# Kernel tuning notes

Measured on AMD Instinct MI355X. Metric: run time of the kernel, lower is better.

Reference implementation:

```python
import jax, jax.numpy as jnp
import numpy as np

# --- static config (matches init_kwargs) ---
B = 2048
N_UP, N_DOWN, N_NUC = 16, 14, 8
N_ELEC = N_UP + N_DOWN            # 30
N_ALL = N_ELEC + N_NUC            # 38
BASIS, KD, ED, L = 32, 64, 128, 3
H_K = int(np.round(np.sqrt(BASIS * KD)))  # 45, log-interp hidden dim of kernel MLP
H_O = int(np.round(np.sqrt(KD * ED)))     # 91, log-interp hidden dim of embed_out MLP

# conv_indexing: all (i, j) pairs with j != i  (i over electrons, j over all particles)
_pairs = np.array([(i, j) for i in range(N_ELEC) for j in range(N_ALL) if j != i], dtype=np.int32)
C_I = jnp.asarray(_pairs[:, 0])
C_J = jnp.asarray(_pairs[:, 1])
P = N_ELEC * (N_ALL - 1)


def ssp(x):
    # shifted softplus: log(0.5*exp(x) + 0.5)
    return jax.nn.softplus(x) - jnp.log(2.0).astype(x.dtype)


def setup_inputs() -> dict:
    key = jax.random.key(0)
    ks = jax.random.split(key, 16)
    # spin-shared electron embeddings (one vector per spin channel, expanded)
    up = jax.random.normal(ks[0], (ED,), jnp.float32)
    dn = jax.random.normal(ks[1], (ED,), jnp.float32)
    embedding_elec = jnp.concatenate([jnp.tile(up, (N_UP, 1)), jnp.tile(dn, (N_DOWN, 1))], axis=0)
    s = 0.1  # weight scale for numerical sanity
    inp = {
        'dists_basis': jax.random.uniform(ks[2], (B, N_ELEC, N_ALL, BASIS), jnp.float32),
        'embedding_elec': embedding_elec,
        'embedding_nuc': jax.random.normal(ks[3], (N_NUC, KD), jnp.float32),
        'kernel_w1': s * jax.random.normal(ks[4], (L, BASIS, H_K), jnp.float32),
        'kernel_b1': s * jax.random.normal(ks[5], (L, H_K), jnp.float32),
        'kernel_w2': s * jax.random.normal(ks[6], (L, H_K, KD), jnp.float32),
        'kernel_b2': s * jax.random.normal(ks[7], (L, KD), jnp.float32),
        'embed_in_w': s * jax.random.normal(ks[8], (L, ED, KD), jnp.float32),
        'out_w1': s * jax.random.normal(ks[9], (L, KD, H_O), jnp.float32),
        'out_b1': s * jax.random.normal(ks[10], (L, H_O), jnp.float32),
        'out_w2': s * jax.random.normal(ks[11], (L, H_O, ED), jnp.float32),
        'out_b2': s * jax.random.normal(ks[12], (L, ED), jnp.float32),
    }
    return inp


def reference(dists_basis, embedding_elec, embedding_nuc, kernel_w1, kernel_b1,
              kernel_w2, kernel_b2, embed_in_w, out_w1, out_b1, out_w2, out_b2):
    b = dists_basis.shape[0]
    # gather all (i,j) pair basis features: (B, P, BASIS)
    db = dists_basis[:, C_I, C_J, :]
    xs = jnp.broadcast_to(embedding_elec, (b, N_ELEC, ED))
    nuc = jnp.broadcast_to(embedding_nuc, (b, N_NUC, KD))
    for l in range(L):  # small fixed number of interaction layers
        # kernel MLP on distance basis -> (B, P, KD)
        Ws = ssp(db @ kernel_w1[l] + kernel_b1[l]) @ kernel_w2[l] + kernel_b2[l]
        # embed_in on electrons, concat nuclei embeddings -> (B, N_ALL, KD)
        zs = jnp.concatenate([xs @ embed_in_w[l], nuc], axis=1)
        # gather neighbors, weight, reduce over neighbor axis -> (B, N_ELEC, KD)
        msg = (Ws * zs[:, C_J]).reshape(b, N_ELEC, N_ALL - 1, KD).sum(axis=2)
        # embed_out MLP -> (B, N_ELEC, ED), residual update
        vs = ssp(msg @ out_w1[l] + out_b1[l]) @ out_w2[l] + out_b2[l]
        xs = xs + vs
    return xs
```

## Files before the change

### kernel.cpp

```cpp
#include <hip/hip_runtime.h>
#include <hip/hip_bf16.h>

typedef __attribute__((ext_vector_type(8))) short bf16x8;
typedef __attribute__((ext_vector_type(4))) float f32x4;
typedef __attribute__((ext_vector_type(16))) float f32x16;
typedef __attribute__((ext_vector_type(2))) unsigned int u32x2;

constexpr int NB = 2048;
constexpr int NE = 30, NN = 8, NAll = 38;
constexpr int BAS = 32, KD = 64, ED = 128, HK = 45, HO = 91, LNUM = 3;

#define MFMA32(a, b, c) __builtin_amdgcn_mfma_f32_32x32x16_bf16((a), (b), (c), 0, 0, 0)

__device__ __forceinline__ unsigned cvtpk(float a, float b) {
    unsigned r;
    asm("v_cvt_pk_bf16_f32 %0, %1, %2" : "=v"(r) : "v"(a), "v"(b));
    return r;
}
__device__ __forceinline__ unsigned short f2b(float v) {
    return (unsigned short)cvtpk(v, v);
}
__device__ __forceinline__ bf16x8 cvt8(f32x4 lo, f32x4 hi) {
    union { unsigned u[4]; bf16x8 v; } r;
    r.u[0] = cvtpk(lo[0], lo[1]);
    r.u[1] = cvtpk(lo[2], lo[3]);
    r.u[2] = cvtpk(hi[0], hi[1]);
    r.u[3] = cvtpk(hi[2], hi[3]);
    return r.v;
}
__device__ __forceinline__ float ssp(float x) {
    float e = __expf(-fabsf(x));
    return fmaxf(x, 0.f) + __logf(fmaf(0.5f, e, 0.5f));
}
__device__ __forceinline__ int swzi(int row, int col, int S) {
    int mask = (S >> 3) - 1;
    int blk = ((col >> 3) ^ row) & mask;
    return row * S + (blk << 3) + (col & 7);
}
__device__ __forceinline__ bf16x8 ldfrag(const unsigned short* p, int S, int row, int col) {
    int mask = (S >> 3) - 1;
    int blk = ((col >> 3) ^ row) & mask;
    return *(const bf16x8*)(p + row * S + (blk << 3));
}
__device__ __forceinline__ f32x4 ldf4s(const float* p, int S, int row, int col) {
    int mask = (S >> 3) - 1;
    int blk = ((col >> 3) ^ row) & mask;
    return *(const f32x4*)(p + row * S + (blk << 3) + (col & 7));
}

__global__ __launch_bounds__(256, 4) void schnet_mfma(
    const float* __restrict__ dists,
    const float* __restrict__ emb_e,
    const float* __restrict__ emb_n,
    const float* __restrict__ kw1, const float* __restrict__ kb1,
    const float* __restrict__ kw2, const float* __restrict__ kb2,
    const float* __restrict__ ew,
    const float* __restrict__ ow1, const float* __restrict__ ob1,
    const float* __restrict__ ow2, const float* __restrict__ ob2,
    float* __restrict__ out)
{
    __shared__ __align__(16) unsigned char smem[26368];
    float* zsb  = (float*)smem;
    float* stot = (float*)(smem + 9728);
    unsigned short* w2t = (unsigned short*)(smem + 9984);
    unsigned char* U = smem + 18176;
    float* msgf = (float*)U;
    unsigned short* hobA = (unsigned short*)U;
    unsigned short* hobB = (unsigned short*)(U + 4096);

    const int b = blockIdx.x;
    const int t = threadIdx.x;
    const int l = t & 63, wv = t >> 6;
    const int li = l & 31, hi = l >> 5;
    const float* db_b = dists + (size_t)b * NE * NAll * BAS;
    float* xsg = out + (size_t)b * NE * ED;
    const int ri = (li < NE) ? li : NE - 1;

    const f32x16 z16 = {0,0,0,0,0,0,0,0,0,0,0,0,0,0,0,0};

    for (int o = t; o < NE * ED; o += 256) xsg[o] = emb_e[o];
    for (int o = t; o < NN * KD; o += 256) zsb[NE * KD + o] = emb_n[o];
    __syncthreads();

    for (int lyr = 0; lyr < LNUM; ++lyr) {
        const float* w1g = kw1 + lyr * BAS * HK;
        const float* b1g = kb1 + lyr * HK;
        const float* w2g = kw2 + lyr * HK * KD;
        const float* b2g = kb2 + lyr * KD;
        const float* weg = ew  + lyr * ED * KD;
        const float* o1g = ow1 + lyr * KD * HO;
        const float* g1g = ob1 + lyr * HO;
        const float* o2g = ow2 + lyr * HO * ED;
        const float* g2g = ob2 + lyr * ED;

        for (int o = t; o < 64 * 64; o += 256) {
            int c = o & 63, h = o >> 6;
            w2t[swzi(c, h, 64)] = f2b((h < HK) ? w2g[h * KD + c] : 0.f);
        }

        bf16x8 w1f[2][2], b1Af[2], oneB;
        {
            #pragma unroll
            for (int T = 0; T < 2; ++T) {
                int h = li + 32 * T;
                bool hv = (h < HK);
                #pragma unroll
                for (int s = 0; s < 2; ++s) {
                    f32x4 lo, hh;
                    #pragma unroll
                    for (int j2 = 0; j2 < 4; ++j2) {
                        int e0 = s * 16 + hi * 8 + j2;
                        lo[j2] = hv ? w1g[e0 * HK + h] : 0.f;
                        hh[j2] = hv ? w1g[(e0 + 4) * HK + h] : 0.f;
                    }
                    w1f[T][s] = cvt8(lo, hh);
                }
                float bv = hv ? b1g[h] : 0.f;
                union { unsigned u[4]; bf16x8 v; } bb;
                bb.u[0] = (hi == 0) ? cvtpk(bv, 0.f) : 0u;
                bb.u[1] = bb.u[2] = bb.u[3] = 0u;
                b1Af[T] = bb.v;
            }
            union { unsigned u[4]; bf16x8 v; } ob;
            ob.u[0] = (hi == 0) ? cvtpk(1.f, 0.f) : 0u;
            ob.u[1] = ob.u[2] = ob.u[3] = 0u;
            oneB = ob.v;
        }

        if (wv < 2) {
            f32x16 zacc = z16;
            #pragma unroll
            for (int s = 0; s < 8; ++s) {
                const float* xp = xsg + ri * ED + s * 16 + hi * 8;
                bf16x8 af = cvt8(*(const f32x4*)xp, *(const f32x4*)(xp + 4));
                f32x4 lo, hh;
                #pragma unroll
                for (int j2 = 0; j2 < 4; ++j2) {
                    int e0 = s * 16 + hi * 8 + j2;
                    lo[j2] = weg[e0 * KD + wv * 32 + li];
                    hh[j2] = weg[(e0 + 4) * KD + wv * 32 + li];
                }
                zacc = MFMA32(af, cvt8(lo, hh), zacc);
            }
            #pragma unroll
            for (int r = 0; r < 16; ++r) {
                int i = (r & 3) + 8 * (r >> 2) + 4 * hi;
                if (i < NE) zsb[i * 64 + wv * 32 + li] = zacc[r];
            }
        }
        __syncthreads();

        if (t < 64) {
            float s = 0.f;
            for (int j2 = 0; j2 < NAll; ++j2) s += zsb[j2 * 64 + t];
            stot[t] = s;
        }
        {
            f32x4 zz4 = {0, 0, 0, 0};
            *(f32x4*)(msgf + t * 8) = zz4;
            *(f32x4*)(msgf + t * 8 + 4) = zz4;
        }

        f32x16 mr0 = z16, mr1 = z16;

        auto pbody = [&](bool DIAG, int j) {
            const float* dp = db_b + (size_t)(ri * NAll + (DIAG ? ri : j)) * BAS + hi * 8;
            bf16x8 fb0 = cvt8(*(const f32x4*)dp, *(const f32x4*)(dp + 4));
            bf16x8 fb1 = cvt8(*(const f32x4*)(dp + 16), *(const f32x4*)(dp + 20));
            f32x16 h0 = MFMA32(b1Af[0], oneB, z16);
            h0 = MFMA32(w1f[0][0], fb0, h0);
            h0 = MFMA32(w1f[0][1], fb1, h0);
            f32x16 h1 = MFMA32(b1Af[1], oneB, z16);
            h1 = MFMA32(w1f[1][0], fb0, h1);
            h1 = MFMA32(w1f[1][1], fb1, h1);
            unsigned d0 = cvtpk(ssp(h0[0]),  ssp(h0[1]));
            unsigned d1 = cvtpk(ssp(h0[2]),  ssp(h0[3]));
            unsigned d2 = cvtpk(ssp(h0[4]),  ssp(h0[5]));
            unsigned d3 = cvtpk(ssp(h0[6]),  ssp(h0[7]));
            unsigned d4 = cvtpk(ssp(h0[8]),  ssp(h0[9]));
            unsigned d5 = cvtpk(ssp(h0[10]), ssp(h0[11]));
            unsigned d6 = cvtpk(ssp(h0[12]), ssp(h0[13]));
            unsigned d7 = cvtpk(ssp(h0[14]), ssp(h0[15]));
            unsigned e0 = cvtpk(ssp(h1[0]),  ssp(h1[1]));
            unsigned e1 = cvtpk(ssp(h1[2]),  ssp(h1[3]));
            unsigned e2 = cvtpk(ssp(h1[4]),  ssp(h1[5]));
            unsigned e3 = cvtpk(ssp(h1[6]),  ssp(h1[7]));
            unsigned pd0 = __shfl_xor(d0, 32, 64), pd1 = __shfl_xor(d1, 32, 64);
            unsigned pd2 = __shfl_xor(d2, 32, 64), pd3 = __shfl_xor(d3, 32, 64);
            unsigned pd4 = __shfl_xor(d4, 32, 64), pd5 = __shfl_xor(d5, 32, 64);
            unsigned pd6 = __shfl_xor(d6, 32, 64), pd7 = __shfl_xor(d7, 32, 64);
            unsigned pe0 = __shfl_xor(e0, 32, 64), pe1 = __shfl_xor(e1, 32, 64);
            unsigned pe2 = __shfl_xor(e2, 32, 64), pe3 = __shfl_xor(e3, 32, 64);
            const bool h0s = (hi == 0);
            union { unsigned u[4]; bf16x8 v; } f0, f1, f2;
            f0.u[0] = h0s ? d0 : pd2;  f0.u[1] = h0s ? d1 : pd3;
            f0.u[2] = h0s ? pd0 : d2;  f0.u[3] = h0s ? pd1 : d3;
            f1.u[0] = h0s ? d4 : pd6;  f1.u[1] = h0s ? d5 : pd7;
            f1.u[2] = h0s ? pd4 : d6;  f1.u[3] = h0s ? pd5 : d7;
            f2.u[0] = h0s ? e0 : pe2;  f2.u[1] = h0s ? e1 : pe3;
            f2.u[2] = h0s ? pe0 : e2;  f2.u[3] = h0s ? pe1 : e3;
            f32x16 a2 = MFMA32(f0.v, ldfrag(w2t, 64, li, hi * 8), z16);
            a2 = MFMA32(f1.v, ldfrag(w2t, 64, li, 16 + hi * 8), a2);
            a2 = MFMA32(f2.v, ldfrag(w2t, 64, li, 32 + hi * 8), a2);
            if (DIAG) {
                #pragma unroll
                for (int r = 0; r < 16; ++r)
                    mr0[r] -= a2[r] * zsb[((r & 3) + 8 * (r >> 2) + 4 * hi) * 64 + li];
            } else {
                float zv = zsb[j * 64 + li];
                #pragma unroll
                for (int r = 0; r < 16; ++r) mr0[r] += a2[r] * zv;
            }
            a2 = MFMA32(f0.v, ldfrag(w2t, 64, 32 + li, hi * 8), z16);
            a2 = MFMA32(f1.v, ldfrag(w2t, 64, 32 + li, 16 + hi * 8), a2);
            a2 = MFMA32(f2.v, ldfrag(w2t, 64, 32 + li, 32 + hi * 8), a2);
            if (DIAG) {
                #pragma unroll
                for (int r = 0; r < 16; ++r)
                    mr1[r] -= a2[r] * zsb[((r & 3) + 8 * (r >> 2) + 4 * hi) * 64 + 32 + li];
            } else {
                float zv = zsb[j * 64 + 32 + li];
                #pragma unroll
                for (int r = 0; r < 16; ++r) mr1[r] += a2[r] * zv;
            }
        };

        for (int j = wv; j < NAll; j += 4) pbody(false, j);
        if (wv == 2) pbody(true, 0);
        __syncthreads();

        if (wv == 3) {
            float b2a = b2g[li], b2b = b2g[32 + li];
            float sta = stot[li], stb = stot[32 + li];
            #pragma unroll
            for (int r = 0; r < 16; ++r) {
                int i = (r & 3) + 8 * (r >> 2) + 4 * hi;
                mr0[r] += b2a * (sta - zsb[i * 64 + li]);
                mr1[r] += b2b * (stb - zsb[i * 64 + 32 + li]);
            }
        }
        #pragma unroll
        for (int r = 0; r < 16; ++r) {
            int i = (r & 3) + 8 * (r >> 2) + 4 * hi;
            atomicAdd(msgf + swzi(i, li, 64), mr0[r]);
            atomicAdd(msgf + swzi(i, 32 + li, 64), mr1[r]);
        }
        __syncthreads();

        f32x16 oacc = z16;
        f32x4 g1q[4];
        if (wv < 3) {
            int h = li + 32 * wv;
            bool hv = (h < HO);
            #pragma unroll
            for (int s = 0; s < 4; ++s) {
                bf16x8 bm = cvt8(ldf4s(msgf, 64, li, s * 16 + hi * 8),
                                 ldf4s(msgf, 64, li, s * 16 + hi * 8 + 4));
                f32x4 lo, hh;
                #pragma unroll
                for (int j2 = 0; j2 < 4; ++j2) {
                    int m = s * 16 + hi * 8 + j2;
                    lo[j2] = hv ? o1g[m * HO + h] : 0.f;
                    hh[j2] = hv ? o1g[(m + 4) * HO + h] : 0.f;
                }
                oacc = MFMA32(cvt8(lo, hh), bm, oacc);
            }
            #pragma unroll
            for (int g = 0; g < 4; ++g)
                #pragma unroll
                for (int j2 = 0; j2 < 4; ++j2) {
                    int h2 = 32 * wv + 8 * g + 4 * hi + j2;
                    g1q[g][j2] = (h2 < HO) ? g1g[h2] : 0.f;
                }
        }
        __syncthreads();
        if (wv < 3) {
            #pragma unroll
            for (int g = 0; g < 4; ++g) {
                u32x2 hv2;
                hv2.x = cvtpk(ssp(oacc[4 * g + 0] + g1q[g][0]), ssp(oacc[4 * g + 1] + g1q[g][1]));
                hv2.y = cvtpk(ssp(oacc[4 * g + 2] + g1q[g][2]), ssp(oacc[4 * g + 3] + g1q[g][3]));
                int colA = 8 * g + 4 * hi;
                if (wv < 2) *(u32x2*)(hobA + swzi(li, 32 * wv + colA, 64)) = hv2;
                else        *(u32x2*)(hobB + swzi(li, colA, 32)) = hv2;
            }
        }
        __syncthreads();
        {
            f32x16 xacc = z16;
            #pragma unroll
            for (int s = 0; s < 6; ++s) {
                bf16x8 af = (s < 4) ? ldfrag(hobA, 64, li, s * 16 + hi * 8)
                                    : ldfrag(hobB, 32, li, (s - 4) * 16 + hi * 8);
                f32x4 lo, hh;
                #pragma unroll
                for (int j2 = 0; j2 < 4; ++j2) {
                    int h2 = s * 16 + hi * 8 + j2;
                    lo[j2] = (h2 < HO) ? o2g[h2 * ED + wv * 32 + li] : 0.f;
                    hh[j2] = (h2 + 4 < HO) ? o2g[(h2 + 4) * ED + wv * 32 + li] : 0.f;
                }
                xacc = MFMA32(af, cvt8(lo, hh), xacc);
            }
            float g2v = g2g[wv * 32 + li];
            #pragma unroll
            for (int r = 0; r < 16; ++r) {
                int i = (r & 3) + 8 * (r >> 2) + 4 * hi;
                if (i < NE) xsg[i * ED + wv * 32 + li] += xacc[r] + g2v;
            }
        }
        __syncthreads();
    }
}

extern "C" void kernel_launch(void* const* d_in, const int* in_sizes, int n_in,
                              void* d_out, int out_size, void* d_ws, size_t ws_size,
                              hipStream_t stream) {
    const float* dists = (const float*)d_in[0];
    const float* emb_e = (const float*)d_in[1];
    const float* emb_n = (const float*)d_in[2];
    const float* kw1   = (const float*)d_in[3];
    const float* kb1   = (const float*)d_in[4];
    const float* kw2   = (const float*)d_in[5];
    const float* kb2   = (const float*)d_in[6];
    const float* ew    = (const float*)d_in[7];
    const float* ow1   = (const float*)d_in[8];
    const float* ob1   = (const float*)d_in[9];
    const float* ow2   = (const float*)d_in[10];
    const float* ob2   = (const float*)d_in[11];
    float* out = (float*)d_out;

    schnet_mfma<<<NB, 256, 0, stream>>>(dists, emb_e, emb_n, kw1, kb1, kw2, kb2,
                                        ew, ow1, ob1, ow2, ob2, out);
}
```

Baseline: 1.481 ms.

## Cache bf16 distance basis in workspace, keep W2 in registers, use permlane swap

On layer 0 the fp32 distance-basis features are converted to bf16 and written to a global workspace, and later layers read the half-size bf16 copy instead of re-reading and re-converting fp32. The kernel-MLP second weight is held as register fragments rather than staged in LDS, which frees shared memory and may allow higher occupancy. The 32-lane cross-half shuffles are replaced with v_permlane32_swap, and the per-pair loads are software-prefetched one iteration ahead. This raises register pressure and adds workspace writes, and the caching path only runs when the harness provides a large enough workspace.

```diff
diff --git a/kernel.cpp b/kernel.cpp
--- a/kernel.cpp
+++ b/kernel.cpp
@@ -16,9 +16,6 @@
     unsigned r;
     asm("v_cvt_pk_bf16_f32 %0, %1, %2" : "=v"(r) : "v"(a), "v"(b));
     return r;
-}
-__device__ __forceinline__ unsigned short f2b(float v) {
-    return (unsigned short)cvtpk(v, v);
 }
 __device__ __forceinline__ bf16x8 cvt8(f32x4 lo, f32x4 hi) {
     union { unsigned u[4]; bf16x8 v; } r;
@@ -31,6 +28,9 @@
 __device__ __forceinline__ float ssp(float x) {
     float e = __expf(-fabsf(x));
     return fmaxf(x, 0.f) + __logf(fmaf(0.5f, e, 0.5f));
+}
+__device__ __forceinline__ void plswap(unsigned& a, unsigned& b) {
+    asm("v_permlane32_swap_b32 %0, %1" : "+v"(a), "+v"(b));
 }
 __device__ __forceinline__ int swzi(int row, int col, int S) {
     int mask = (S >> 3) - 1;
@@ -57,13 +57,13 @@
     const float* __restrict__ ew,
     const float* __restrict__ ow1, const float* __restrict__ ob1,
     const float* __restrict__ ow2, const float* __restrict__ ob2,
-    float* __restrict__ out)
+    float* __restrict__ out,
+    unsigned short* __restrict__ wsb, int useb)
 {
-    __shared__ __align__(16) unsigned char smem[26368];
+    __shared__ __align__(16) unsigned char smem[18176];
     float* zsb  = (float*)smem;
     float* stot = (float*)(smem + 9728);
-    unsigned short* w2t = (unsigned short*)(smem + 9984);
-    unsigned char* U = smem + 18176;
+    unsigned char* U = smem + 9984;
     float* msgf = (float*)U;
     unsigned short* hobA = (unsigned short*)U;
     unsigned short* hobB = (unsigned short*)(U + 4096);
@@ -73,6 +73,7 @@
     const int l = t & 63, wv = t >> 6;
     const int li = l & 31, hi = l >> 5;
     const float* db_b = dists + (size_t)b * NE * NAll * BAS;
+    unsigned short* ws_b = wsb + (size_t)b * NE * NAll * BAS;
     float* xsg = out + (size_t)b * NE * ED;
     const int ri = (li < NE) ? li : NE - 1;
 
@@ -93,12 +94,7 @@
         const float* o2g = ow2 + lyr * HO * ED;
         const float* g2g = ob2 + lyr * ED;
 
-        for (int o = t; o < 64 * 64; o += 256) {
-            int c = o & 63, h = o >> 6;
-            w2t[swzi(c, h, 64)] = f2b((h < HK) ? w2g[h * KD + c] : 0.f);
-        }
-
-        bf16x8 w1f[2][2], b1Af[2], oneB;
+        bf16x8 w1f[2][2], b1Af[2], oneB, w2f[6];
         {
             #pragma unroll
             for (int T = 0; T < 2; ++T) {
@@ -125,6 +121,20 @@
             ob.u[0] = (hi == 0) ? cvtpk(1.f, 0.f) : 0u;
             ob.u[1] = ob.u[2] = ob.u[3] = 0u;
             oneB = ob.v;
+            #pragma unroll
+            for (int cb = 0; cb < 2; ++cb)
+                #pragma unroll
+                for (int s = 0; s < 3; ++s) {
+                    int c = cb * 32 + li;
+                    f32x4 lo, hh;
+                    #pragma unroll
+                    for (int j2 = 0; j2 < 4; ++j2) {
+                        int h = s * 16 + hi * 8 + j2;
+                        lo[j2] = (h < HK) ? w2g[h * KD + c] : 0.f;
+                        hh[j2] = (h + 4 < HK) ? w2g[(h + 4) * KD + c] : 0.f;
+                    }
+                    w2f[cb * 3 + s] = cvt8(lo, hh);
+                }
         }
 
         if (wv < 2) {
@@ -163,10 +173,7 @@
 
         f32x16 mr0 = z16, mr1 = z16;
 
-        auto pbody = [&](bool DIAG, int j) {
-            const float* dp = db_b + (size_t)(ri * NAll + (DIAG ? ri : j)) * BAS + hi * 8;
-            bf16x8 fb0 = cvt8(*(const f32x4*)dp, *(const f32x4*)(dp + 4));
-            bf16x8 fb1 = cvt8(*(const f32x4*)(dp + 16), *(const f32x4*)(dp + 20));
+        auto pcompute = [&](bool DIAG, int j, bf16x8 fb0, bf16x8 fb1) {
             f32x16 h0 = MFMA32(b1Af[0], oneB, z16);
             h0 = MFMA32(w1f[0][0], fb0, h0);
             h0 = MFMA32(w1f[0][1], fb1, h0);
@@ -185,23 +192,15 @@
             unsigned e1 = cvtpk(ssp(h1[2]),  ssp(h1[3]));
             unsigned e2 = cvtpk(ssp(h1[4]),  ssp(h1[5]));
             unsigned e3 = cvtpk(ssp(h1[6]),  ssp(h1[7]));
-            unsigned pd0 = __shfl_xor(d0, 32, 64), pd1 = __shfl_xor(d1, 32, 64);
-            unsigned pd2 = __shfl_xor(d2, 32, 64), pd3 = __shfl_xor(d3, 32, 64);
-            unsigned pd4 = __shfl_xor(d4, 32, 64), pd5 = __shfl_xor(d5, 32, 64);
-            unsigned pd6 = __shfl_xor(d6, 32, 64), pd7 = __shfl_xor(d7, 32, 64);
-            unsigned pe0 = __shfl_xor(e0, 32, 64), pe1 = __shfl_xor(e1, 32, 64);
-            unsigned pe2 = __shfl_xor(e2, 32, 64), pe3 = __shfl_xor(e3, 32, 64);
-            const bool h0s = (hi == 0);
-            union { unsigned u[4]; bf16x8 v; } f0, f1, f2;
-            f0.u[0] = h0s ? d0 : pd2;  f0.u[1] = h0s ? d1 : pd3;
-            f0.u[2] = h0s ? pd0 : d2;  f0.u[3] = h0s ? pd1 : d3;
-            f1.u[0] = h0s ? d4 : pd6;  f1.u[1] = h0s ? d5 : pd7;
-            f1.u[2] = h0s ? pd4 : d6;  f1.u[3] = h0s ? pd5 : d7;
-            f2.u[0] = h0s ? e0 : pe2;  f2.u[1] = h0s ? e1 : pe3;
-            f2.u[2] = h0s ? pe0 : e2;  f2.u[3] = h0s ? pe1 : e3;
-            f32x16 a2 = MFMA32(f0.v, ldfrag(w2t, 64, li, hi * 8), z16);
-            a2 = MFMA32(f1.v, ldfrag(w2t, 64, li, 16 + hi * 8), a2);
-            a2 = MFMA32(f2.v, ldfrag(w2t, 64, li, 32 + hi * 8), a2);
+            plswap(d0, d2); plswap(d1, d3);
+            plswap(d4, d6); plswap(d5, d7);
+            plswap(e0, e2); plswap(e1, e3);
+            union { unsigned u[4]; bf16x8 v; } f0 = {{d0, d1, d2, d3}},
+                                               f1 = {{d4, d5, d6, d7}},
+                                               f2 = {{e0, e1, e2, e3}};
+            f32x16 a2 = MFMA32(f0.v, w2f[0], z16);
+            a2 = MFMA32(f1.v, w2f[1], a2);
+            a2 = MFMA32(f2.v, w2f[2], a2);
             if (DIAG) {
                 #pragma unroll
                 for (int r = 0; r < 16; ++r)
@@ -211,9 +210,9 @@
                 #pragma unroll
                 for (int r = 0; r < 16; ++r) mr0[r] += a2[r] * zv;
             }
-            a2 = MFMA32(f0.v, ldfrag(w2t, 64, 32 + li, hi * 8), z16);
-            a2 = MFMA32(f1.v, ldfrag(w2t, 64, 32 + li, 16 + hi * 8), a2);
-            a2 = MFMA32(f2.v, ldfrag(w2t, 64, 32 + li, 32 + hi * 8), a2);
+            a2 = MFMA32(f0.v, w2f[3], z16);
+            a2 = MFMA32(f1.v, w2f[4], a2);
+            a2 = MFMA32(f2.v, w2f[5], a2);
             if (DIAG) {
                 #pragma unroll
                 for (int r = 0; r < 16; ++r)
@@ -225,8 +224,52 @@
             }
         };
 
-        for (int j = wv; j < NAll; j += 4) pbody(false, j);
-        if (wv == 2) pbody(true, 0);
+        if (useb && lyr > 0) {
+            const unsigned short* p0 = ws_b + ((size_t)ri * NAll + wv) * BAS + hi * 8;
+            const unsigned short* p1 = p0 + 4 * BAS;
+            bf16x8 A0 = *(const bf16x8*)p0, A1 = *(const bf16x8*)(p0 + 16);
+            bf16x8 B0 = *(const bf16x8*)p1, B1 = *(const bf16x8*)(p1 + 16);
+            for (int j = wv; j < NAll; j += 4) {
+                bf16x8 C0 = B0, C1 = B1;
+                if (j + 8 < NAll) {
+                    const unsigned short* pn = ws_b + ((size_t)ri * NAll + j + 8) * BAS + hi * 8;
+                    C0 = *(const bf16x8*)pn; C1 = *(const bf16x8*)(pn + 16);
+                }
+                pcompute(false, j, A0, A1);
+                A0 = B0; A1 = B1; B0 = C0; B1 = C1;
+            }
+        } else {
+            const float* dp0 = db_b + ((size_t)ri * NAll + wv) * BAS + hi * 8;
+            f32x4 cA = *(const f32x4*)dp0, cB = *(const f32x4*)(dp0 + 4);
+            f32x4 cC = *(const f32x4*)(dp0 + 16), cD = *(const f32x4*)(dp0 + 20);
+            for (int j = wv; j < NAll; j += 4) {
+                f32x4 nA = cA, nB = cB, nC = cC, nD = cD;
+                if (j + 4 < NAll) {
+                    const float* dp = db_b + ((size_t)ri * NAll + j + 4) * BAS + hi * 8;
+                    nA = *(const f32x4*)dp;        nB = *(const f32x4*)(dp + 4);
+                    nC = *(const f32x4*)(dp + 16); nD = *(const f32x4*)(dp + 20);
+                }
+                bf16x8 fb0 = cvt8(cA, cB), fb1 = cvt8(cC, cD);
+                if (useb) {
+                    unsigned short* wp = ws_b + ((size_t)ri * NAll + j) * BAS + hi * 8;
+                    *(bf16x8*)wp = fb0; *(bf16x8*)(wp + 16) = fb1;
+                }
+                pcompute(false, j, fb0, fb1);
+                cA = nA; cB = nB; cC = nC; cD = nD;
+            }
+        }
+        if (wv == 2) {
+            bf16x8 g0, g1;
+            if (useb && lyr > 0) {
+                const unsigned short* p = ws_b + ((size_t)ri * NAll + ri) * BAS + hi * 8;
+                g0 = *(const bf16x8*)p; g1 = *(const bf16x8*)(p + 16);
+            } else {
+                const float* dp = db_b + ((size_t)ri * NAll + ri) * BAS + hi * 8;
+                g0 = cvt8(*(const f32x4*)dp, *(const f32x4*)(dp + 4));
+                g1 = cvt8(*(const f32x4*)(dp + 16), *(const f32x4*)(dp + 20));
+            }
+            pcompute(true, 0, g0, g1);
+        }
         __syncthreads();
 
         if (wv == 3) {
@@ -329,6 +372,10 @@
     const float* ob2   = (const float*)d_in[11];
     float* out = (float*)d_out;
 
+    const size_t need = (size_t)NB * NE * NAll * BAS * sizeof(unsigned short);
+    int useb = (d_ws != nullptr && ws_size >= need) ? 1 : 0;
+
     schnet_mfma<<<NB, 256, 0, stream>>>(dists, emb_e, emb_n, kw1, kb1, kw2, kb2,
-                                        ew, ow1, ob1, ow2, ob2, out);
-}
+                                        ew, ow1, ob1, ow2, ob2, out,
+                                        (unsigned short*)d_ws, useb);
+}
```

Result: slower. 1.650 ms (+11.3%).
